# Kernel tuning notes

Measured on AMD Instinct MI355X. Metric: run time of the kernel, lower is better.

The kernel has to match this reference:

```python
import jax, jax.numpy as jnp
import numpy as np

NHEAD = 8
LN_EPS = 1e-5


def _layernorm(x, g, b):
    mu = jnp.mean(x, -1, keepdims=True)
    var = jnp.mean((x - mu) ** 2, -1, keepdims=True)
    return (x - mu) / jnp.sqrt(var + LN_EPS) * g + b


def _sparse_attn(q, k, v, P):
    # Topology: P queries attend to P keys; G queries attend to P keys + self.
    # q,k,v: [B,H,L,dh], keys/values restricted to pcpt block [B,H,P,dh]
    dh = q.shape[-1]
    scale = 1.0 / jnp.sqrt(jnp.asarray(dh, q.dtype))
    kp, vp = k[:, :, :P], v[:, :, :P]
    S = jnp.einsum('bhld,bhpd->bhlp', q, kp) * scale  # [B,H,L,P]
    # pcpt queries: plain softmax over P keys
    out_p = jnp.einsum('bhqp,bhpd->bhqd', jax.nn.softmax(S[:, :, :P], axis=-1), vp)
    # gen queries: P keys + own diagonal key
    qg, kg, vg = q[:, :, P:], k[:, :, P:], v[:, :, P:]
    Sg = S[:, :, P:]                                   # [B,H,G,P]
    dlog = jnp.sum(qg * kg, -1) * scale                # [B,H,G] diagonal logits
    m = jnp.maximum(jnp.max(Sg, -1), dlog)
    eg = jnp.exp(Sg - m[..., None])
    ed = jnp.exp(dlog - m)
    den = jnp.sum(eg, -1) + ed
    out_g = (jnp.einsum('bhgp,bhpd->bhgd', eg, vp) + ed[..., None] * vg) / den[..., None]
    return jnp.concatenate([out_p, out_g], axis=2)     # [B,H,L,dh]


def _forward(pcpt, gen, Wqkv, bqkv, Wo, bo, W1, b1, W2, b2, g1, beta1, g2, beta2):
    P = pcpt.shape[1]
    x = jnp.concatenate([pcpt, gen], axis=1)           # [B,L,d]
    B, L, d = x.shape
    dh = d // NHEAD
    for i in range(Wqkv.shape[0]):  # post-norm layers
        qkv = (x @ Wqkv[i] + bqkv[i]).reshape(B, L, 3, NHEAD, dh)
        q = jnp.transpose(qkv[:, :, 0], (0, 2, 1, 3))
        k = jnp.transpose(qkv[:, :, 1], (0, 2, 1, 3))
        v = jnp.transpose(qkv[:, :, 2], (0, 2, 1, 3))
        a = _sparse_attn(q, k, v, P)
        a = jnp.transpose(a, (0, 2, 1, 3)).reshape(B, L, d)
        a = a @ Wo[i] + bo[i]
        x = _layernorm(x + a, g1[i], beta1[i])
        h = jax.nn.relu(x @ W1[i] + b1[i]) @ W2[i] + b2[i]
        x = _layernorm(x + h, g2[i], beta2[i])
    return x


def setup_inputs() -> dict:
    key = jax.random.key(0)
    ks = jax.random.split(key, 16)
    B, P, G, d, ff, Lyr = 4, 1024, 1024, 512, 2048, 4
    s = 0.02
    f32 = jnp.float32
    return {
        'pcpt_total_embs': jax.random.normal(ks[0], (B, P, d), f32),
        'gen_total_embs': jax.random.normal(ks[1], (B, G, d), f32),
        'src_key_padding_mask': jnp.zeros((B, P + G), bool),
        'Wqkv': jax.random.normal(ks[2], (Lyr, d, 3 * d), f32) * s,
        'bqkv': jnp.zeros((Lyr, 3 * d), f32),
        'Wo': jax.random.normal(ks[3], (Lyr, d, d), f32) * s,
        'bo': jnp.zeros((Lyr, d), f32),
        'W1': jax.random.normal(ks[4], (Lyr, d, ff), f32) * s,
        'b1': jnp.zeros((Lyr, ff), f32),
        'W2': jax.random.normal(ks[5], (Lyr, ff, d), f32) * s,
        'b2': jnp.zeros((Lyr, d), f32),
        'g1': jnp.ones((Lyr, d), f32),
        'beta1': jnp.zeros((Lyr, d), f32),
        'g2': jnp.ones((Lyr, d), f32),
        'beta2': jnp.zeros((Lyr, d), f32),
    }


def reference(pcpt_total_embs, gen_total_embs, src_key_padding_mask, Wqkv, bqkv, Wo, bo, W1, b1, W2, b2, g1, beta1, g2, beta2):
    P = pcpt_total_embs.shape[1]
    x = _forward(pcpt_total_embs, gen_total_embs, Wqkv, bqkv, Wo, bo, W1, b1, W2, b2, g1, beta1, g2, beta2)
    return x[:, :P], x[:, P:]
```

## Files before the change

kernel.cpp:

```cpp
#include <hip/hip_runtime.h>
#include <hip/hip_bf16.h>

#define B_ 4
#define P_ 1024
#define G_ 1024
#define L_ 2048
#define D_ 512
#define FF_ 2048
#define H_ 8
#define DH_ 64
#define LAYERS_ 4
#define LN_EPS_ 1e-5f

typedef __attribute__((ext_vector_type(8))) short bf16x8;
typedef __attribute__((ext_vector_type(4))) float f32x4;

__device__ __forceinline__ ushort f2b(float f) {
  unsigned u = __float_as_uint(f);
  unsigned r = (u + 0x7fffu + ((u >> 16) & 1u)) >> 16;
  return (ushort)r;
}
__device__ __forceinline__ float b2f(ushort u) {
  return __uint_as_float(((unsigned)u) << 16);
}

__device__ __forceinline__ void gld16(const ushort* g, ushort* l) {
  __builtin_amdgcn_global_load_lds(
      (const __attribute__((address_space(1))) void*)g,
      (__attribute__((address_space(3))) void*)l, 16, 0, 0);
}

__global__ __launch_bounds__(256) void concat_kernel(const float* __restrict__ p,
    const float* __restrict__ g, float* __restrict__ x, ushort* __restrict__ xb)
{
  const int LD4 = L_*D_/4, PD4 = P_*D_/4;
  int i = blockIdx.x*256 + threadIdx.x;
  int b = i / LD4, r = i - b*LD4;
  float4 v;
  if (r < PD4) v = ((const float4*)p)[(size_t)b*PD4 + r];
  else         v = ((const float4*)g)[(size_t)b*PD4 + (r-PD4)];
  ((float4*)x)[i] = v;
  ushort4 h; h.x=f2b(v.x); h.y=f2b(v.y); h.z=f2b(v.z); h.w=f2b(v.w);
  ((ushort4*)xb)[i] = h;
}

__global__ __launch_bounds__(256) void writeout_kernel(const float* __restrict__ x,
    float* __restrict__ out)
{
  const int LD4 = L_*D_/4, PD4 = P_*D_/4, HALF = B_*PD4;
  int i = blockIdx.x*256 + threadIdx.x;
  int half = (i >= HALF) ? 1 : 0;
  int r = i - half*HALF;
  int b = r / PD4, q = r - b*PD4;
  ((float4*)out)[i] = ((const float4*)x)[(size_t)b*LD4 + half*PD4 + q];
}

__global__ __launch_bounds__(256) void wconv_kernel(const float* __restrict__ src,
    ushort* __restrict__ dst, int K, int N)
{
  __shared__ float tile[32][33];
  int n0 = blockIdx.x*32, k0 = blockIdx.y*32, l = blockIdx.z;
  src += (size_t)l*K*N; dst += (size_t)l*K*N;
  int tx = threadIdx.x & 31, ty = threadIdx.x >> 5;
  #pragma unroll
  for (int u=0;u<4;++u) tile[ty+8*u][tx] = src[(size_t)(k0+ty+8*u)*N + n0+tx];
  __syncthreads();
  #pragma unroll
  for (int u=0;u<4;++u) dst[(size_t)(n0+ty+8*u)*K + k0+tx] = f2b(tile[tx][ty+8*u]);
}

template<int BN_, int RELU, int RES, int OUTBF>
__global__ __launch_bounds__(256) void mgemm(
    const ushort* __restrict__ A, const ushort* __restrict__ Bt,
    const float* __restrict__ bias, const float* __restrict__ res,
    void* __restrict__ Cout, int M, int N, int K)
{
  constexpr int MI = (BN_ == 128) ? 4 : 2;
  constexpr int BL = BN_ / 32;
  __shared__ ushort As[128*64];
  __shared__ ushort Bs[BN_*64];
  int t = threadIdx.x;
  int lane = t & 63, w = t >> 6;
  int wm = (BN_ == 128) ? (w >> 1) * 64 : w * 32;
  int wn = (BN_ == 128) ? (w & 1) * 64 : 0;
  int m0 = blockIdx.x * 128, n0 = blockIdx.y * BN_;

  f32x4 acc[MI][4] = {};

  int rbase = t >> 3;
  int cch   = (t & 7) ^ ((t >> 3) & 7);
  const ushort* Ag = A  + (size_t)(m0 + rbase)*K + cch*8;
  const ushort* Bg = Bt + (size_t)(n0 + rbase)*K + cch*8;
  ushort* Asl = As + t*8;
  ushort* Bsl = Bs + t*8;
  const size_t rowK32 = (size_t)32 * K;

  int fr = lane & 15, fq = lane >> 4;
  int swr[2];
  swr[0] = ((0*4 + fq) ^ (fr & 7)) * 8;
  swr[1] = ((1*4 + fq) ^ (fr & 7)) * 8;
  const ushort* Ard = As + (wm + fr)*64;
  const ushort* Brd = Bs + (wn + fr)*64;

  for (int k0 = 0; k0 < K; k0 += 64) {
    __syncthreads();
    #pragma unroll
    for (int L = 0; L < 4; ++L)  gld16(Ag + L*rowK32, Asl + L*2048);
    #pragma unroll
    for (int L = 0; L < BL; ++L) gld16(Bg + L*rowK32, Bsl + L*2048);
    Ag += 64; Bg += 64;
    __syncthreads();
    #pragma unroll
    for (int s = 0; s < 2; ++s) {
      int sw = swr[s];
      bf16x8 af[MI], bfr[4];
      #pragma unroll
      for (int i=0;i<MI;++i) af[i]  = *(const bf16x8*)(Ard + i*16*64 + sw);
      #pragma unroll
      for (int j=0;j<4;++j)  bfr[j] = *(const bf16x8*)(Brd + j*16*64 + sw);
      #pragma unroll
      for (int i=0;i<MI;++i)
        #pragma unroll
        for (int j=0;j<4;++j)
          acc[i][j] = __builtin_amdgcn_mfma_f32_16x16x32_bf16(af[i], bfr[j], acc[i][j], 0, 0, 0);
    }
  }

  int ncol = lane & 15;
  int rquad = (lane >> 4) * 4;
  #pragma unroll
  for (int j=0;j<4;++j) {
    int n = n0 + wn + j*16 + ncol;
    float bv = bias[n];
    #pragma unroll
    for (int i=0;i<MI;++i) {
      int mbase = m0 + wm + i*16 + rquad;
      #pragma unroll
      for (int r=0;r<4;++r) {
        int m = mbase + r;
        float c = acc[i][j][r] + bv;
        if (RES) c += res[(size_t)m*N + n];
        if (RELU) c = fmaxf(c, 0.f);
        if (OUTBF) ((ushort*)Cout)[(size_t)m*N + n] = f2b(c);
        else       ((float*)Cout)[(size_t)m*N + n] = c;
      }
    }
  }
}

__global__ __launch_bounds__(256) void mgemm_qkv(
    const ushort* __restrict__ A,
    const ushort* __restrict__ Bt,
    const float* __restrict__ bias,
    ushort* __restrict__ qb,
    ushort* __restrict__ kb,
    ushort* __restrict__ vtb)
{
  const int K = D_;
  __shared__ ushort As[128*64];
  __shared__ ushort Bs[128*64];
  int t = threadIdx.x;
  int lane = t & 63, w = t >> 6;
  int wm = (w >> 1) * 64, wn = (w & 1) * 64;
  int m0 = blockIdx.x * 128, n0 = blockIdx.y * 128;

  f32x4 acc[4][4] = {};

  int rbase = t >> 3;
  int cch   = (t & 7) ^ ((t >> 3) & 7);
  const ushort* Ag = A  + (size_t)(m0 + rbase)*K + cch*8;
  const ushort* Bg = Bt + (size_t)(n0 + rbase)*K + cch*8;
  ushort* Asl = As + t*8;
  ushort* Bsl = Bs + t*8;
  const size_t rowK32 = (size_t)32 * K;

  int fr = lane & 15, fq = lane >> 4;
  int swr[2];
  swr[0] = ((0*4 + fq) ^ (fr & 7)) * 8;
  swr[1] = ((1*4 + fq) ^ (fr & 7)) * 8;
  const ushort* Ard = As + (wm + fr)*64;
  const ushort* Brd = Bs + (wn + fr)*64;

  for (int k0 = 0; k0 < K; k0 += 64) {
    __syncthreads();
    #pragma unroll
    for (int L = 0; L < 4; ++L) gld16(Ag + L*rowK32, Asl + L*2048);
    #pragma unroll
    for (int L = 0; L < 4; ++L) gld16(Bg + L*rowK32, Bsl + L*2048);
    Ag += 64; Bg += 64;
    __syncthreads();
    #pragma unroll
    for (int s = 0; s < 2; ++s) {
      int sw = swr[s];
      bf16x8 af[4], bfr[4];
      #pragma unroll
      for (int i=0;i<4;++i) af[i]  = *(const bf16x8*)(Ard + i*16*64 + sw);
      #pragma unroll
      for (int j=0;j<4;++j) bfr[j] = *(const bf16x8*)(Brd + j*16*64 + sw);
      #pragma unroll
      for (int i=0;i<4;++i)
        #pragma unroll
        for (int j=0;j<4;++j)
          acc[i][j] = __builtin_amdgcn_mfma_f32_16x16x32_bf16(af[i], bfr[j], acc[i][j], 0, 0, 0);
    }
  }

  int ncol = lane & 15;
  int rquad = (lane >> 4) * 4;
  #pragma unroll
  for (int j=0;j<4;++j) {
    int n = n0 + wn + j*16 + ncol;
    float bv = bias[n];
    int part = n >> 9;
    int wi = n & 511;
    int h = wi >> 6, d = wi & 63;
    #pragma unroll
    for (int i=0;i<4;++i) {
      int mbase = m0 + wm + i*16 + rquad;
      #pragma unroll
      for (int r=0;r<4;++r) {
        int m = mbase + r;
        int b = m >> 11, l = m & 2047;
        int bh = b*H_ + h;
        float cv = acc[i][j][r] + bv;
        if (part == 0) cv *= 0.125f;
        ushort c = f2b(cv);
        if (part == 0)      qb[((size_t)bh*L_ + l)*DH_ + d] = c;
        else if (part == 1) kb[((size_t)bh*L_ + l)*DH_ + d] = c;
        else                vtb[((size_t)bh*DH_ + d)*L_ + l] = c;
      }
    }
  }
}

__global__ __launch_bounds__(256) void attn_mfma(
    const ushort* __restrict__ qb, const ushort* __restrict__ kb,
    const ushort* __restrict__ vtb, ushort* __restrict__ outa)
{
  __shared__ ushort Qs[64*72];
  __shared__ ushort Ks[64*72];
  __shared__ ushort Vts[64*72];
  __shared__ ushort Ps[4*16*72];
  __shared__ float dls[64];

  int t = threadIdx.x;
  int lane = t & 63, w = t >> 6;
  int qt = blockIdx.x & 31;
  int h  = (blockIdx.x >> 5) & 7;
  int b  = blockIdx.x >> 8;
  int l0 = qt * 64;
  bool isgen = (l0 >= P_);
  int bh = b*H_ + h;

  const ushort* qg  = qb  + ((size_t)bh*L_ + l0)*DH_;
  const ushort* kgb = kb  + (size_t)bh*L_*DH_;
  const ushort* vtg = vtb + (size_t)bh*DH_*L_;

  int sr = t >> 3, sc = (t & 7) * 8;

  {
    uint4 x0 = *(const uint4*)(qg + (size_t)sr*DH_ + sc);
    uint4 x1 = *(const uint4*)(qg + (size_t)(sr+32)*DH_ + sc);
    *(uint4*)(Qs + sr*72 + sc) = x0;
    *(uint4*)(Qs + (sr+32)*72 + sc) = x1;
  }
  __syncthreads();

  int fr = lane & 15, fq = lane >> 4;
  bf16x8 qf[2];
  qf[0] = *(const bf16x8*)(Qs + (16*w + fr)*72 + 0*32 + fq*8);
  qf[1] = *(const bf16x8*)(Qs + (16*w + fr)*72 + 1*32 + fq*8);

  float den[4] = {0.f, 0.f, 0.f, 0.f};
  f32x4 o[4] = {};

  ushort* Pw = Ps + w*16*72;

  uint4 pk0 = *(const uint4*)(kgb + (size_t)sr*DH_ + sc);
  uint4 pk1 = *(const uint4*)(kgb + (size_t)(sr+32)*DH_ + sc);
  uint4 pv0 = *(const uint4*)(vtg + (size_t)sr*L_ + sc);
  uint4 pv1 = *(const uint4*)(vtg + (size_t)(sr+32)*L_ + sc);

  for (int kt = 0; kt < 16; ++kt) {
    __syncthreads();
    *(uint4*)(Ks + sr*72 + sc) = pk0;
    *(uint4*)(Ks + (sr+32)*72 + sc) = pk1;
    *(uint4*)(Vts + sr*72 + sc) = pv0;
    *(uint4*)(Vts + (sr+32)*72 + sc) = pv1;
    __syncthreads();

    if (kt < 15) {
      int p1 = (kt + 1) * 64;
      pk0 = *(const uint4*)(kgb + (size_t)(p1+sr)*DH_ + sc);
      pk1 = *(const uint4*)(kgb + (size_t)(p1+sr+32)*DH_ + sc);
      pv0 = *(const uint4*)(vtg + (size_t)sr*L_ + p1 + sc);
      pv1 = *(const uint4*)(vtg + (size_t)(sr+32)*L_ + p1 + sc);
    }

    f32x4 sc4[4] = {};
    #pragma unroll
    for (int s=0;s<2;++s) {
      #pragma unroll
      for (int j=0;j<4;++j) {
        bf16x8 kf = *(const bf16x8*)(Ks + (j*16 + fr)*72 + s*32 + fq*8);
        sc4[j] = __builtin_amdgcn_mfma_f32_16x16x32_bf16(qf[s], kf, sc4[j], 0, 0, 0);
      }
    }

    #pragma unroll
    for (int r=0;r<4;++r) {
      float e0 = __expf(sc4[0][r]);
      float e1 = __expf(sc4[1][r]);
      float e2 = __expf(sc4[2][r]);
      float e3 = __expf(sc4[3][r]);
      den[r] += (e0+e1) + (e2+e3);
      Pw[(fq*4+r)*72 +  0 + fr] = (ushort)(__float_as_uint(e0) >> 16);
      Pw[(fq*4+r)*72 + 16 + fr] = (ushort)(__float_as_uint(e1) >> 16);
      Pw[(fq*4+r)*72 + 32 + fr] = (ushort)(__float_as_uint(e2) >> 16);
      Pw[(fq*4+r)*72 + 48 + fr] = (ushort)(__float_as_uint(e3) >> 16);
    }
    asm volatile("s_waitcnt lgkmcnt(0)" ::: "memory");

    #pragma unroll
    for (int s=0;s<2;++s) {
      bf16x8 pf = *(const bf16x8*)(Pw + fr*72 + s*32 + fq*8);
      #pragma unroll
      for (int j=0;j<4;++j) {
        bf16x8 vf = *(const bf16x8*)(Vts + (j*16 + fr)*72 + s*32 + fq*8);
        o[j] = __builtin_amdgcn_mfma_f32_16x16x32_bf16(pf, vf, o[j], 0, 0, 0);
      }
    }
  }

  #pragma unroll
  for (int r=0;r<4;++r) {
    float d = den[r];
    d += __shfl_xor(d, 1, 16);
    d += __shfl_xor(d, 2, 16);
    d += __shfl_xor(d, 4, 16);
    d += __shfl_xor(d, 8, 16);
    den[r] = d;
  }

  if (isgen) {
    __syncthreads();
    {
      uint4 k0v = *(const uint4*)(kgb + (size_t)(l0+sr)*DH_ + sc);
      uint4 k1v = *(const uint4*)(kgb + (size_t)(l0+sr+32)*DH_ + sc);
      uint4 v0v = *(const uint4*)(vtg + (size_t)sr*L_ + l0 + sc);
      uint4 v1v = *(const uint4*)(vtg + (size_t)(sr+32)*L_ + l0 + sc);
      *(uint4*)(Ks + sr*72 + sc) = k0v;
      *(uint4*)(Ks + (sr+32)*72 + sc) = k1v;
      *(uint4*)(Vts + sr*72 + sc) = v0v;
      *(uint4*)(Vts + (sr+32)*72 + sc) = v1v;
    }
    __syncthreads();
    {
      int row = t >> 2, part = t & 3;
      float dsum = 0.f;
      #pragma unroll
      for (int u=0;u<16;++u) {
        int d = part*16 + u;
        dsum = fmaf(b2f(Qs[row*72+d]), b2f(Ks[row*72+d]), dsum);
      }
      dsum += __shfl_xor(dsum, 1, 4);
      dsum += __shfl_xor(dsum, 2, 4);
      if (part == 0) dls[row] = dsum;
    }
    __syncthreads();
    #pragma unroll
    for (int r=0;r<4;++r) {
      int rr = 16*w + fq*4 + r;
      float ed = __expf(dls[rr]);
      den[r] += ed;
      #pragma unroll
      for (int j=0;j<4;++j) {
        float vv = b2f(Vts[(j*16 + fr)*72 + rr]);
        o[j][r] += ed*vv;
      }
    }
  }

  #pragma unroll
  for (int r=0;r<4;++r) {
    float inv = 1.f / den[r];
    int l = l0 + 16*w + fq*4 + r;
    #pragma unroll
    for (int j=0;j<4;++j)
      outa[((size_t)b*L_ + l)*D_ + h*DH_ + j*16 + fr] = f2b(o[j][r]*inv);
  }
}

__global__ __launch_bounds__(64) void ln_kernel(const float* __restrict__ y,
    const float* __restrict__ gw, const float* __restrict__ bw,
    float* __restrict__ x, ushort* __restrict__ xb)
{
  int row = blockIdx.x, t = threadIdx.x;
  const float4* yr = (const float4*)(y + (size_t)row*D_);
  float4 v0 = yr[t], v1 = yr[t+64];
  float s = v0.x+v0.y+v0.z+v0.w + v1.x+v1.y+v1.z+v1.w;
  for (int off=32; off>0; off>>=1) s += __shfl_down(s, off, 64);
  s = __shfl(s, 0, 64);
  float mu = s * (1.f/D_);
  float dx;
  float q = 0.f;
  dx=v0.x-mu; q+=dx*dx; dx=v0.y-mu; q+=dx*dx; dx=v0.z-mu; q+=dx*dx; dx=v0.w-mu; q+=dx*dx;
  dx=v1.x-mu; q+=dx*dx; dx=v1.y-mu; q+=dx*dx; dx=v1.z-mu; q+=dx*dx; dx=v1.w-mu; q+=dx*dx;
  for (int off=32; off>0; off>>=1) q += __shfl_down(q, off, 64);
  q = __shfl(q, 0, 64);
  float rinv = rsqrtf(q*(1.f/D_) + LN_EPS_);
  const float4* g4 = (const float4*)gw;
  const float4* b4 = (const float4*)bw;
  float4 gv0=g4[t], gv1=g4[t+64], bv0=b4[t], bv1=b4[t+64];
  float4 o0, o1;
  o0.x=(v0.x-mu)*rinv*gv0.x+bv0.x; o0.y=(v0.y-mu)*rinv*gv0.y+bv0.y;
  o0.z=(v0.z-mu)*rinv*gv0.z+bv0.z; o0.w=(v0.w-mu)*rinv*gv0.w+bv0.w;
  o1.x=(v1.x-mu)*rinv*gv1.x+bv1.x; o1.y=(v1.y-mu)*rinv*gv1.y+bv1.y;
  o1.z=(v1.z-mu)*rinv*gv1.z+bv1.z; o1.w=(v1.w-mu)*rinv*gv1.w+bv1.w;
  float4* xr = (float4*)(x + (size_t)row*D_);
  xr[t]=o0; xr[t+64]=o1;
  ushort4 h0, h1;
  h0.x=f2b(o0.x); h0.y=f2b(o0.y); h0.z=f2b(o0.z); h0.w=f2b(o0.w);
  h1.x=f2b(o1.x); h1.y=f2b(o1.y); h1.z=f2b(o1.z); h1.w=f2b(o1.w);
  ushort4* xbr = (ushort4*)(xb + (size_t)row*D_);
  xbr[t]=h0; xbr[t+64]=h1;
}

extern "C" void kernel_launch(void* const* d_in, const int* in_sizes, int n_in,
                              void* d_out, int out_size, void* d_ws, size_t ws_size,
                              hipStream_t stream) {
  const float* pcpt = (const float*)d_in[0];
  const float* gen  = (const float*)d_in[1];
  const float* Wqkv = (const float*)d_in[3];
  const float* bqkv = (const float*)d_in[4];
  const float* Wo   = (const float*)d_in[5];
  const float* bo   = (const float*)d_in[6];
  const float* W1   = (const float*)d_in[7];
  const float* b1   = (const float*)d_in[8];
  const float* W2   = (const float*)d_in[9];
  const float* b2   = (const float*)d_in[10];
  const float* g1   = (const float*)d_in[11];
  const float* be1  = (const float*)d_in[12];
  const float* g2   = (const float*)d_in[13];
  const float* be2  = (const float*)d_in[14];
  float* out = (float*)d_out;

  const size_t XD  = (size_t)B_*L_*D_;
  const size_t HKV = (size_t)B_*H_*L_*DH_;
  const size_t HFF = (size_t)B_*L_*FF_;

  float*  xbuf = (float*)d_ws;
  ushort* xbf  = (ushort*)(xbuf + XD);
  ushort* region = xbf + XD;
  ushort* qb  = region;
  ushort* kb  = region + HKV;
  ushort* vtb = region + 2*HKV;
  ushort* hbf = region;
  ushort* abf = region + HFF;
  ushort* wb  = abf + XD;
  ushort* wqkv_b = wb;
  ushort* wo_b   = wqkv_b + (size_t)4*3*D_*D_;
  ushort* w1_b   = wo_b   + (size_t)4*D_*D_;
  ushort* w2_b   = w1_b   + (size_t)4*FF_*D_;
  float*  ybuf = out;

  const int M = B_*L_;

  wconv_kernel<<<dim3(3*D_/32, D_/32, 4), 256, 0, stream>>>(Wqkv, wqkv_b, D_, 3*D_);
  wconv_kernel<<<dim3(D_/32,   D_/32, 4), 256, 0, stream>>>(Wo,   wo_b,   D_, D_);
  wconv_kernel<<<dim3(FF_/32,  D_/32, 4), 256, 0, stream>>>(W1,   w1_b,   D_, FF_);
  wconv_kernel<<<dim3(D_/32,  FF_/32, 4), 256, 0, stream>>>(W2,   w2_b,   FF_, D_);

  concat_kernel<<<4096, 256, 0, stream>>>(pcpt, gen, xbuf, xbf);

  for (int i = 0; i < LAYERS_; ++i) {
    const ushort* wqkv_i = wqkv_b + (size_t)i*3*D_*D_;
    const ushort* wo_i   = wo_b   + (size_t)i*D_*D_;
    const ushort* w1_i   = w1_b   + (size_t)i*FF_*D_;
    const ushort* w2_i   = w2_b   + (size_t)i*D_*FF_;
    const float* bqkv_i = bqkv + (size_t)i*3*D_;
    const float* bo_i   = bo   + (size_t)i*D_;
    const float* b1_i   = b1   + (size_t)i*FF_;
    const float* b2_i   = b2   + (size_t)i*D_;
    const float* g1_i   = g1   + (size_t)i*D_;
    const float* be1_i  = be1  + (size_t)i*D_;
    const float* g2_i   = g2   + (size_t)i*D_;
    const float* be2_i  = be2  + (size_t)i*D_;

    mgemm_qkv<<<dim3(M/128, 3*D_/128), 256, 0, stream>>>(
        xbf, wqkv_i, bqkv_i, qb, kb, vtb);

    attn_mfma<<<B_*H_*(L_/64), 256, 0, stream>>>(qb, kb, vtb, abf);

    mgemm<64,0,1,0><<<dim3(M/128, D_/64), 256, 0, stream>>>(
        abf, wo_i, bo_i, xbuf, ybuf, M, D_, D_);

    ln_kernel<<<M, 64, 0, stream>>>(ybuf, g1_i, be1_i, xbuf, xbf);

    mgemm<128,1,0,1><<<dim3(M/128, FF_/128), 256, 0, stream>>>(
        xbf, w1_i, b1_i, nullptr, hbf, M, FF_, D_);

    mgemm<64,0,1,0><<<dim3(M/128, D_/64), 256, 0, stream>>>(
        hbf, w2_i, b2_i, xbuf, ybuf, M, D_, FF_);

    ln_kernel<<<M, 64, 0, stream>>>(ybuf, g2_i, be2_i, xbuf, xbf);
  }

  writeout_kernel<<<4096, 256, 0, stream>>>(xbuf, out);
}
```

Before: 795.9 us.

## Split-K the FFN down-projection, swizzle attention LDS, use exp2 softmax

After: 798.0 us. About the same (+0.3%).

```diff
diff --git a/kernel.cpp b/kernel.cpp
--- a/kernel.cpp
+++ b/kernel.cpp
@@ -148,6 +148,82 @@
   }
 }
 
+__global__ __launch_bounds__(256) void mgemm_sk(
+    const ushort* __restrict__ A, const ushort* __restrict__ Bt,
+    const float* __restrict__ bias, float* __restrict__ C0,
+    float* __restrict__ C1, int M, int N, int K)
+{
+  __shared__ ushort As[128*64];
+  __shared__ ushort Bs[64*64];
+  int t = threadIdx.x;
+  int lane = t & 63, w = t >> 6;
+  int wm = w * 32, wn = 0;
+  int m0 = blockIdx.x * 128, n0 = blockIdx.y * 64;
+  int slice = blockIdx.z;
+  int Kh = K >> 1;
+  const ushort* Ab = A  + slice*Kh;
+  const ushort* Bb = Bt + slice*Kh;
+  float* C = slice ? C1 : C0;
+
+  f32x4 acc[2][4] = {};
+
+  int rbase = t >> 3;
+  int cch   = (t & 7) ^ ((t >> 3) & 7);
+  const ushort* Ag = Ab + (size_t)(m0 + rbase)*K + cch*8;
+  const ushort* Bg = Bb + (size_t)(n0 + rbase)*K + cch*8;
+  ushort* Asl = As + t*8;
+  ushort* Bsl = Bs + t*8;
+  const size_t rowK32 = (size_t)32 * K;
+
+  int fr = lane & 15, fq = lane >> 4;
+  int swr[2];
+  swr[0] = ((0*4 + fq) ^ (fr & 7)) * 8;
+  swr[1] = ((1*4 + fq) ^ (fr & 7)) * 8;
+  const ushort* Ard = As + (wm + fr)*64;
+  const ushort* Brd = Bs + (wn + fr)*64;
+
+  for (int k0 = 0; k0 < Kh; k0 += 64) {
+    __syncthreads();
+    #pragma unroll
+    for (int L = 0; L < 4; ++L) gld16(Ag + L*rowK32, Asl + L*2048);
+    #pragma unroll
+    for (int L = 0; L < 2; ++L) gld16(Bg + L*rowK32, Bsl + L*2048);
+    Ag += 64; Bg += 64;
+    __syncthreads();
+    #pragma unroll
+    for (int s = 0; s < 2; ++s) {
+      int sw = swr[s];
+      bf16x8 af[2], bfr[4];
+      #pragma unroll
+      for (int i=0;i<2;++i) af[i]  = *(const bf16x8*)(Ard + i*16*64 + sw);
+      #pragma unroll
+      for (int j=0;j<4;++j) bfr[j] = *(const bf16x8*)(Brd + j*16*64 + sw);
+      #pragma unroll
+      for (int i=0;i<2;++i)
+        #pragma unroll
+        for (int j=0;j<4;++j)
+          acc[i][j] = __builtin_amdgcn_mfma_f32_16x16x32_bf16(af[i], bfr[j], acc[i][j], 0, 0, 0);
+    }
+  }
+
+  int ncol = lane & 15;
+  int rquad = (lane >> 4) * 4;
+  #pragma unroll
+  for (int j=0;j<4;++j) {
+    int n = n0 + wn + j*16 + ncol;
+    float bv = slice ? 0.f : bias[n];
+    #pragma unroll
+    for (int i=0;i<2;++i) {
+      int mbase = m0 + wm + i*16 + rquad;
+      #pragma unroll
+      for (int r=0;r<4;++r) {
+        int m = mbase + r;
+        C[(size_t)m*N + n] = acc[i][j][r] + bv;
+      }
+    }
+  }
+}
+
 __global__ __launch_bounds__(256) void mgemm_qkv(
     const ushort* __restrict__ A,
     const ushort* __restrict__ Bt,
@@ -223,7 +299,7 @@
         int b = m >> 11, l = m & 2047;
         int bh = b*H_ + h;
         float cv = acc[i][j][r] + bv;
-        if (part == 0) cv *= 0.125f;
+        if (part == 0) cv *= 0.18033688f;
         ushort c = f2b(cv);
         if (part == 0)      qb[((size_t)bh*L_ + l)*DH_ + d] = c;
         else if (part == 1) kb[((size_t)bh*L_ + l)*DH_ + d] = c;
@@ -237,10 +313,10 @@
     const ushort* __restrict__ qb, const ushort* __restrict__ kb,
     const ushort* __restrict__ vtb, ushort* __restrict__ outa)
 {
-  __shared__ ushort Qs[64*72];
-  __shared__ ushort Ks[64*72];
-  __shared__ ushort Vts[64*72];
-  __shared__ ushort Ps[4*16*72];
+  __shared__ ushort Qs[64*64];
+  __shared__ ushort Ks[64*64];
+  __shared__ ushort Vts[64*64];
+  __shared__ ushort Ps[4*16*64];
   __shared__ float dls[64];
 
   int t = threadIdx.x;
@@ -256,45 +332,51 @@
   const ushort* kgb = kb  + (size_t)bh*L_*DH_;
   const ushort* vtg = vtb + (size_t)bh*DH_*L_;
 
-  int sr = t >> 3, sc = (t & 7) * 8;
+  int sr = t >> 3;
+  int ct = t & 7;
+  int gcol = ct * 8;
+  int scol = (ct ^ (sr & 7)) * 8;
 
   {
-    uint4 x0 = *(const uint4*)(qg + (size_t)sr*DH_ + sc);
-    uint4 x1 = *(const uint4*)(qg + (size_t)(sr+32)*DH_ + sc);
-    *(uint4*)(Qs + sr*72 + sc) = x0;
-    *(uint4*)(Qs + (sr+32)*72 + sc) = x1;
+    uint4 x0 = *(const uint4*)(qg + (size_t)sr*DH_ + gcol);
+    uint4 x1 = *(const uint4*)(qg + (size_t)(sr+32)*DH_ + gcol);
+    *(uint4*)(Qs + sr*64 + scol) = x0;
+    *(uint4*)(Qs + (sr+32)*64 + scol) = x1;
   }
   __syncthreads();
 
   int fr = lane & 15, fq = lane >> 4;
+  int fsw[2];
+  fsw[0] = ((0*4 + fq) ^ (fr & 7)) * 8;
+  fsw[1] = ((1*4 + fq) ^ (fr & 7)) * 8;
   bf16x8 qf[2];
-  qf[0] = *(const bf16x8*)(Qs + (16*w + fr)*72 + 0*32 + fq*8);
-  qf[1] = *(const bf16x8*)(Qs + (16*w + fr)*72 + 1*32 + fq*8);
+  qf[0] = *(const bf16x8*)(Qs + (16*w + fr)*64 + fsw[0]);
+  qf[1] = *(const bf16x8*)(Qs + (16*w + fr)*64 + fsw[1]);
 
   float den[4] = {0.f, 0.f, 0.f, 0.f};
   f32x4 o[4] = {};
 
-  ushort* Pw = Ps + w*16*72;
-
-  uint4 pk0 = *(const uint4*)(kgb + (size_t)sr*DH_ + sc);
-  uint4 pk1 = *(const uint4*)(kgb + (size_t)(sr+32)*DH_ + sc);
-  uint4 pv0 = *(const uint4*)(vtg + (size_t)sr*L_ + sc);
-  uint4 pv1 = *(const uint4*)(vtg + (size_t)(sr+32)*L_ + sc);
+  ushort* Pw = Ps + w*16*64;
+
+  uint4 pk0 = *(const uint4*)(kgb + (size_t)sr*DH_ + gcol);
+  uint4 pk1 = *(const uint4*)(kgb + (size_t)(sr+32)*DH_ + gcol);
+  uint4 pv0 = *(const uint4*)(vtg + (size_t)sr*L_ + gcol);
+  uint4 pv1 = *(const uint4*)(vtg + (size_t)(sr+32)*L_ + gcol);
 
   for (int kt = 0; kt < 16; ++kt) {
     __syncthreads();
-    *(uint4*)(Ks + sr*72 + sc) = pk0;
-    *(uint4*)(Ks + (sr+32)*72 + sc) = pk1;
-    *(uint4*)(Vts + sr*72 + sc) = pv0;
-    *(uint4*)(Vts + (sr+32)*72 + sc) = pv1;
+    *(uint4*)(Ks + sr*64 + scol) = pk0;
+    *(uint4*)(Ks + (sr+32)*64 + scol) = pk1;
+    *(uint4*)(Vts + sr*64 + scol) = pv0;
+    *(uint4*)(Vts + (sr+32)*64 + scol) = pv1;
     __syncthreads();
 
     if (kt < 15) {
       int p1 = (kt + 1) * 64;
-      pk0 = *(const uint4*)(kgb + (size_t)(p1+sr)*DH_ + sc);
-      pk1 = *(const uint4*)(kgb + (size_t)(p1+sr+32)*DH_ + sc);
-      pv0 = *(const uint4*)(vtg + (size_t)sr*L_ + p1 + sc);
-      pv1 = *(const uint4*)(vtg + (size_t)(sr+32)*L_ + p1 + sc);
+      pk0 = *(const uint4*)(kgb + (size_t)(p1+sr)*DH_ + gcol);
+      pk1 = *(const uint4*)(kgb + (size_t)(p1+sr+32)*DH_ + gcol);
+      pv0 = *(const uint4*)(vtg + (size_t)sr*L_ + p1 + gcol);
+      pv1 = *(const uint4*)(vtg + (size_t)(sr+32)*L_ + p1 + gcol);
     }
 
     f32x4 sc4[4] = {};
@@ -302,31 +384,34 @@
     for (int s=0;s<2;++s) {
       #pragma unroll
       for (int j=0;j<4;++j) {
-        bf16x8 kf = *(const bf16x8*)(Ks + (j*16 + fr)*72 + s*32 + fq*8);
+        bf16x8 kf = *(const bf16x8*)(Ks + (j*16 + fr)*64 + fsw[s]);
         sc4[j] = __builtin_amdgcn_mfma_f32_16x16x32_bf16(qf[s], kf, sc4[j], 0, 0, 0);
       }
     }
 
     #pragma unroll
     for (int r=0;r<4;++r) {
-      float e0 = __expf(sc4[0][r]);
-      float e1 = __expf(sc4[1][r]);
-      float e2 = __expf(sc4[2][r]);
-      float e3 = __expf(sc4[3][r]);
+      float e0 = exp2f(sc4[0][r]);
+      float e1 = exp2f(sc4[1][r]);
+      float e2 = exp2f(sc4[2][r]);
+      float e3 = exp2f(sc4[3][r]);
       den[r] += (e0+e1) + (e2+e3);
-      Pw[(fq*4+r)*72 +  0 + fr] = (ushort)(__float_as_uint(e0) >> 16);
-      Pw[(fq*4+r)*72 + 16 + fr] = (ushort)(__float_as_uint(e1) >> 16);
-      Pw[(fq*4+r)*72 + 32 + fr] = (ushort)(__float_as_uint(e2) >> 16);
-      Pw[(fq*4+r)*72 + 48 + fr] = (ushort)(__float_as_uint(e3) >> 16);
+      int rr = fq*4 + r;
+      int rx = (rr & 7);
+      int wi = fr & 7, hi = fr >> 3;
+      Pw[rr*64 + (((0 + hi) ^ rx)*8) + wi] = (ushort)(__float_as_uint(e0) >> 16);
+      Pw[rr*64 + (((2 + hi) ^ rx)*8) + wi] = (ushort)(__float_as_uint(e1) >> 16);
+      Pw[rr*64 + (((4 + hi) ^ rx)*8) + wi] = (ushort)(__float_as_uint(e2) >> 16);
+      Pw[rr*64 + (((6 + hi) ^ rx)*8) + wi] = (ushort)(__float_as_uint(e3) >> 16);
     }
     asm volatile("s_waitcnt lgkmcnt(0)" ::: "memory");
 
     #pragma unroll
     for (int s=0;s<2;++s) {
-      bf16x8 pf = *(const bf16x8*)(Pw + fr*72 + s*32 + fq*8);
+      bf16x8 pf = *(const bf16x8*)(Pw + fr*64 + fsw[s]);
       #pragma unroll
       for (int j=0;j<4;++j) {
-        bf16x8 vf = *(const bf16x8*)(Vts + (j*16 + fr)*72 + s*32 + fq*8);
+        bf16x8 vf = *(const bf16x8*)(Vts + (j*16 + fr)*64 + fsw[s]);
         o[j] = __builtin_amdgcn_mfma_f32_16x16x32_bf16(pf, vf, o[j], 0, 0, 0);
       }
     }
@@ -345,23 +430,25 @@
   if (isgen) {
     __syncthreads();
     {
-      uint4 k0v = *(const uint4*)(kgb + (size_t)(l0+sr)*DH_ + sc);
-      uint4 k1v = *(const uint4*)(kgb + (size_t)(l0+sr+32)*DH_ + sc);
-      uint4 v0v = *(const uint4*)(vtg + (size_t)sr*L_ + l0 + sc);
-      uint4 v1v = *(const uint4*)(vtg + (size_t)(sr+32)*L_ + l0 + sc);
-      *(uint4*)(Ks + sr*72 + sc) = k0v;
-      *(uint4*)(Ks + (sr+32)*72 + sc) = k1v;
-      *(uint4*)(Vts + sr*72 + sc) = v0v;
-      *(uint4*)(Vts + (sr+32)*72 + sc) = v1v;
+      uint4 k0v = *(const uint4*)(kgb + (size_t)(l0+sr)*DH_ + gcol);
+      uint4 k1v = *(const uint4*)(kgb + (size_t)(l0+sr+32)*DH_ + gcol);
+      uint4 v0v = *(const uint4*)(vtg + (size_t)sr*L_ + l0 + gcol);
+      uint4 v1v = *(const uint4*)(vtg + (size_t)(sr+32)*L_ + l0 + gcol);
+      *(uint4*)(Ks + sr*64 + scol) = k0v;
+      *(uint4*)(Ks + (sr+32)*64 + scol) = k1v;
+      *(uint4*)(Vts + sr*64 + scol) = v0v;
+      *(uint4*)(Vts + (sr+32)*64 + scol) = v1v;
     }
     __syncthreads();
     {
       int row = t >> 2, part = t & 3;
+      int rx = row & 7;
       float dsum = 0.f;
       #pragma unroll
       for (int u=0;u<16;++u) {
         int d = part*16 + u;
-        dsum = fmaf(b2f(Qs[row*72+d]), b2f(Ks[row*72+d]), dsum);
+        int idx = row*64 + (((d>>3) ^ rx)*8) + (d&7);
+        dsum = fmaf(b2f(Qs[idx]), b2f(Ks[idx]), dsum);
       }
       dsum += __shfl_xor(dsum, 1, 4);
       dsum += __shfl_xor(dsum, 2, 4);
@@ -371,11 +458,11 @@
     #pragma unroll
     for (int r=0;r<4;++r) {
       int rr = 16*w + fq*4 + r;
-      float ed = __expf(dls[rr]);
+      float ed = exp2f(dls[rr]);
       den[r] += ed;
       #pragma unroll
       for (int j=0;j<4;++j) {
-        float vv = b2f(Vts[(j*16 + fr)*72 + rr]);
+        float vv = b2f(Vts[(j*16 + fr)*64 + (((rr>>3) ^ (fr & 7))*8) + (rr & 7)]);
         o[j][r] += ed*vv;
       }
     }
@@ -426,6 +513,48 @@
   xbr[t]=h0; xbr[t+64]=h1;
 }
 
+__global__ __launch_bounds__(64) void ln2_kernel(const float* __restrict__ y0,
+    const float* __restrict__ y1, const float* __restrict__ xres,
+    const float* __restrict__ gw, const float* __restrict__ bw,
+    float* __restrict__ x, ushort* __restrict__ xb)
+{
+  int row = blockIdx.x, t = threadIdx.x;
+  const float4* a4 = (const float4*)(y0 + (size_t)row*D_);
+  const float4* c4 = (const float4*)(y1 + (size_t)row*D_);
+  const float4* r4 = (const float4*)(xres + (size_t)row*D_);
+  float4 v0 = a4[t], v1 = a4[t+64];
+  float4 u0 = c4[t], u1 = c4[t+64];
+  float4 w0 = r4[t], w1 = r4[t+64];
+  v0.x+=u0.x+w0.x; v0.y+=u0.y+w0.y; v0.z+=u0.z+w0.z; v0.w+=u0.w+w0.w;
+  v1.x+=u1.x+w1.x; v1.y+=u1.y+w1.y; v1.z+=u1.z+w1.z; v1.w+=u1.w+w1.w;
+  float s = v0.x+v0.y+v0.z+v0.w + v1.x+v1.y+v1.z+v1.w;
+  for (int off=32; off>0; off>>=1) s += __shfl_down(s, off, 64);
+  s = __shfl(s, 0, 64);
+  float mu = s * (1.f/D_);
+  float dx;
+  float q = 0.f;
+  dx=v0.x-mu; q+=dx*dx; dx=v0.y-mu; q+=dx*dx; dx=v0.z-mu; q+=dx*dx; dx=v0.w-mu; q+=dx*dx;
+  dx=v1.x-mu; q+=dx*dx; dx=v1.y-mu; q+=dx*dx; dx=v1.z-mu; q+=dx*dx; dx=v1.w-mu; q+=dx*dx;
+  for (int off=32; off>0; off>>=1) q += __shfl_down(q, off, 64);
+  q = __shfl(q, 0, 64);
+  float rinv = rsqrtf(q*(1.f/D_) + LN_EPS_);
+  const float4* g4 = (const float4*)gw;
+  const float4* b4 = (const float4*)bw;
+  float4 gv0=g4[t], gv1=g4[t+64], bv0=b4[t], bv1=b4[t+64];
+  float4 o0, o1;
+  o0.x=(v0.x-mu)*rinv*gv0.x+bv0.x; o0.y=(v0.y-mu)*rinv*gv0.y+bv0.y;
+  o0.z=(v0.z-mu)*rinv*gv0.z+bv0.z; o0.w=(v0.w-mu)*rinv*gv0.w+bv0.w;
+  o1.x=(v1.x-mu)*rinv*gv1.x+bv1.x; o1.y=(v1.y-mu)*rinv*gv1.y+bv1.y;
+  o1.z=(v1.z-mu)*rinv*gv1.z+bv1.z; o1.w=(v1.w-mu)*rinv*gv1.w+bv1.w;
+  float4* xr = (float4*)(x + (size_t)row*D_);
+  xr[t]=o0; xr[t+64]=o1;
+  ushort4 h0, h1;
+  h0.x=f2b(o0.x); h0.y=f2b(o0.y); h0.z=f2b(o0.z); h0.w=f2b(o0.w);
+  h1.x=f2b(o1.x); h1.y=f2b(o1.y); h1.z=f2b(o1.z); h1.w=f2b(o1.w);
+  ushort4* xbr = (ushort4*)(xb + (size_t)row*D_);
+  xbr[t]=h0; xbr[t+64]=h1;
+}
+
 extern "C" void kernel_launch(void* const* d_in, const int* in_sizes, int n_in,
                               void* d_out, int out_size, void* d_ws, size_t ws_size,
                               hipStream_t stream) {
@@ -462,6 +591,7 @@
   ushort* wo_b   = wqkv_b + (size_t)4*3*D_*D_;
   ushort* w1_b   = wo_b   + (size_t)4*D_*D_;
   ushort* w2_b   = w1_b   + (size_t)4*FF_*D_;
+  float*  ypart1 = (float*)(w2_b + (size_t)4*D_*FF_);
   float*  ybuf = out;
 
   const int M = B_*L_;
@@ -500,10 +630,10 @@
     mgemm<128,1,0,1><<<dim3(M/128, FF_/128), 256, 0, stream>>>(
         xbf, w1_i, b1_i, nullptr, hbf, M, FF_, D_);
 
-    mgemm<64,0,1,0><<<dim3(M/128, D_/64), 256, 0, stream>>>(
-        hbf, w2_i, b2_i, xbuf, ybuf, M, D_, FF_);
-
-    ln_kernel<<<M, 64, 0, stream>>>(ybuf, g2_i, be2_i, xbuf, xbf);
+    mgemm_sk<<<dim3(M/128, D_/64, 2), 256, 0, stream>>>(
+        hbf, w2_i, b2_i, ybuf, ypart1, M, D_, FF_);
+
+    ln2_kernel<<<M, 64, 0, stream>>>(ybuf, ypart1, xbuf, g2_i, be2_i, xbuf, xbf);
   }
 
   writeout_kernel<<<4096, 256, 0, stream>>>(xbuf, out);
```
